# Kernel optimization log

Measured on AMD Instinct MI355X. Metric: run time of the kernel, lower is better.

Reference implementation:

```python
import jax, jax.numpy as jnp
import numpy as np

D_MODEL = 1024
NUM_HEADS = 16
D_K = D_MODEL // NUM_HEADS
THETA = 10000.0
B, S = 2, 2048


def apply_rope(x, token_position, theta=THETA):
    # x: [B, H, S, d_k]; token_position: [B, S] int
    d_k = x.shape[-1]
    inv_freq = 1.0 / theta ** (jnp.arange(0, d_k, 2, dtype=jnp.float32) / d_k)  # [d_k/2]
    angles = token_position.astype(jnp.float32)[:, :, None] * inv_freq[None, None, :]  # [B,S,d_k/2]
    cos = jnp.cos(angles)[:, None, :, :]  # [B,1,S,d_k/2]
    sin = jnp.sin(angles)[:, None, :, :]
    x_even = x[..., 0::2]
    x_odd = x[..., 1::2]
    rot_even = x_even * cos - x_odd * sin
    rot_odd = x_even * sin + x_odd * cos
    # interleave back: stack on new last axis, then flatten
    return jnp.stack([rot_even, rot_odd], axis=-1).reshape(x.shape)


def setup_inputs() -> dict:
    key = jax.random.key(0)
    kx, kq, kk, kv, ko = jax.random.split(key, 5)
    scale = 1.0 / np.sqrt(D_MODEL)
    x = jax.random.normal(kx, (B, S, D_MODEL), dtype=jnp.float32)
    WQ = jax.random.normal(kq, (D_MODEL, D_MODEL), dtype=jnp.float32) * scale
    WK = jax.random.normal(kk, (D_MODEL, D_MODEL), dtype=jnp.float32) * scale
    WV = jax.random.normal(kv, (D_MODEL, D_MODEL), dtype=jnp.float32) * scale
    WO = jax.random.normal(ko, (D_MODEL, D_MODEL), dtype=jnp.float32) * scale
    token_position = jnp.broadcast_to(jnp.arange(S, dtype=jnp.int32)[None, :], (B, S))
    return {"x": x, "token_position": token_position, "WQ": WQ, "WK": WK, "WV": WV, "WO": WO}


def reference(x, token_position, WQ, WK, WV, WO):
    Batch, seq, _ = x.shape
    Q = jnp.einsum('bsd,de->bse', x, WQ).reshape(Batch, seq, NUM_HEADS, D_K).transpose(0, 2, 1, 3)
    K = jnp.einsum('bsd,de->bse', x, WK).reshape(Batch, seq, NUM_HEADS, D_K).transpose(0, 2, 1, 3)
    V = jnp.einsum('bsd,de->bse', x, WV).reshape(Batch, seq, NUM_HEADS, D_K).transpose(0, 2, 1, 3)
    Q = apply_rope(Q, token_position)
    K = apply_rope(K, token_position)
    score = jnp.einsum('bhqd,bhkd->bhqk', Q, K) / jnp.sqrt(jnp.float32(D_K))
    causal = jnp.tril(jnp.ones((seq, seq), dtype=bool))  # [S,S]
    score = jnp.where(causal[None, None, :, :], score, -jnp.inf)
    probs = jax.nn.softmax(score, axis=-1)
    out = jnp.einsum('bhqk,bhkd->bhqd', probs, V)
    out = out.transpose(0, 2, 1, 3).reshape(Batch, seq, D_MODEL)
    return jnp.einsum('bsd,de->bse', out, WO)
```

## Files before the change

### kernel.cpp

```cpp
#include <hip/hip_runtime.h>
#include <hip/hip_bf16.h>

typedef __attribute__((ext_vector_type(8))) short short8;
typedef __attribute__((ext_vector_type(4))) float f32x4;
typedef __hip_bfloat16 bf16_t;

#define SEQ 2048
#define DM 1024
#define NH 16
#define DK 64

static __device__ __forceinline__ f32x4 mfma16x16x32(short8 a, short8 b, f32x4 c) {
  return __builtin_amdgcn_mfma_f32_16x16x32_bf16(a, b, c, 0, 0, 0);
}

__global__ void sniff_dtype(const unsigned int* __restrict__ x, int* __restrict__ flag) {
  int lane = threadIdx.x & 63;
  int cnt = 0;
  for (int r = 0; r < 4; ++r) {
    unsigned int v = x[lane + r * 64];
    int e = (v >> 7) & 0xFF;
    if (e >= 100 && e <= 145) cnt++;
  }
  for (int d = 1; d < 64; d <<= 1) cnt += __shfl_xor(cnt, d, 64);
  if (lane == 0) *flag = (cnt >= 192) ? 1 : 0;
}

__global__ __launch_bounds__(256) void prep(const void* __restrict__ x,
                                            bf16_t* __restrict__ Xc,
                                            const void* __restrict__ w0,
                                            const void* __restrict__ w1,
                                            const void* __restrict__ w2,
                                            const void* __restrict__ w3,
                                            bf16_t* __restrict__ wt_base,
                                            const int* __restrict__ tokpos,
                                            float2* __restrict__ rtab,
                                            const int* __restrict__ flag) {
  int f = *flag;
  int bx = blockIdx.x, t = threadIdx.x;
  __shared__ bf16_t tile[64][65];
  if (bx < 4096) {
    int i = bx * 256 + t;
    if (f) {
      ((uint2*)Xc)[i] = ((const uint2*)x)[i];
    } else {
      const float4 v = ((const float4*)x)[i];
      bf16_t o[4] = {__float2bfloat16(v.x), __float2bfloat16(v.y),
                     __float2bfloat16(v.z), __float2bfloat16(v.w)};
      ((uint2*)Xc)[i] = *(const uint2*)o;
    }
  } else if (bx < 5120) {
    int rem = bx - 4096;
    int z = rem >> 8, bxx = rem & 15, byy = (rem >> 4) & 15;
    const void* src = (z == 0) ? w0 : (z == 1) ? w1 : (z == 2) ? w2 : w3;
    bf16_t* dst = wt_base + (size_t)((z + 1) & 3) * DM * DM;
    int tx = t & 63, ty = t >> 6;
    int r0 = byy * 64, c0 = bxx * 64;
    for (int i = 0; i < 64; i += 4) {
      size_t idx = (size_t)(r0 + ty + i) * DM + c0 + tx;
      tile[ty + i][tx] = f ? ((const bf16_t*)src)[idx]
                           : __float2bfloat16(((const float*)src)[idx]);
    }
    __syncthreads();
    for (int i = 0; i < 64; i += 4)
      dst[(size_t)(c0 + ty + i) * DM + r0 + tx] = tile[tx][ty + i];
  } else {
    int i = (bx - 5120) * 256 + t;
    int m = i >> 5, pp = i & 31;
    float pos = (float)tokpos[m];
    float invf = __powf(10000.0f, -(float)pp * (1.0f / 32.0f));
    float sn, cs;
    sincosf(pos * invf, &sn, &cs);
    rtab[i] = make_float2(cs, sn);
  }
}

__global__ __launch_bounds__(256) void gemm128_qkv(const bf16_t* __restrict__ A,
                                                   const bf16_t* __restrict__ WTqkv,
                                                   bf16_t* __restrict__ Qb,
                                                   bf16_t* __restrict__ Kb,
                                                   bf16_t* __restrict__ VTo,
                                                   const float2* __restrict__ rtab) {
  __shared__ __align__(16) char smem[36864];
  bf16_t (*As)[72] = (bf16_t(*)[72])smem;
  bf16_t (*Bs)[72] = (bf16_t(*)[72])(smem + 18432);
  int t = threadIdx.x;
  int w = t >> 6, lane = t & 63, l15 = lane & 15, quad = lane >> 4;
  int wrow = w >> 1, wcol = w & 1;
  int m0 = blockIdx.y * 128, nx = blockIdx.x, n0 = nx * 128;
  int srow = t >> 1, scol = (t & 1) * 32;
  const bf16_t* ag = A + (size_t)(m0 + srow) * DM + scol;
  const bf16_t* bg = WTqkv + (size_t)(n0 + srow) * DM + scol;
  f32x4 acc[4][4] = {};
  for (int kk = 0; kk < DM; kk += 64) {
    short8 a0 = *(const short8*)(ag + kk);
    short8 a1 = *(const short8*)(ag + kk + 8);
    short8 a2 = *(const short8*)(ag + kk + 16);
    short8 a3 = *(const short8*)(ag + kk + 24);
    short8 b0 = *(const short8*)(bg + kk);
    short8 b1 = *(const short8*)(bg + kk + 8);
    short8 b2 = *(const short8*)(bg + kk + 16);
    short8 b3 = *(const short8*)(bg + kk + 24);
    __syncthreads();
    *(short8*)&As[srow][scol] = a0;       *(short8*)&As[srow][scol + 8] = a1;
    *(short8*)&As[srow][scol + 16] = a2;  *(short8*)&As[srow][scol + 24] = a3;
    *(short8*)&Bs[srow][scol] = b0;       *(short8*)&Bs[srow][scol + 8] = b1;
    *(short8*)&Bs[srow][scol + 16] = b2;  *(short8*)&Bs[srow][scol + 24] = b3;
    __syncthreads();
    short8 af[4][2], bfr[4][2];
#pragma unroll
    for (int mt = 0; mt < 4; ++mt) {
      af[mt][0] = *(const short8*)&As[wrow * 64 + mt * 16 + l15][quad * 8];
      af[mt][1] = *(const short8*)&As[wrow * 64 + mt * 16 + l15][32 + quad * 8];
    }
#pragma unroll
    for (int nt = 0; nt < 4; ++nt) {
      bfr[nt][0] = *(const short8*)&Bs[wcol * 64 + nt * 16 + l15][quad * 8];
      bfr[nt][1] = *(const short8*)&Bs[wcol * 64 + nt * 16 + l15][32 + quad * 8];
    }
#pragma unroll
    for (int mt = 0; mt < 4; ++mt)
#pragma unroll
      for (int nt = 0; nt < 4; ++nt) {
        acc[mt][nt] = mfma16x16x32(af[mt][0], bfr[nt][0], acc[mt][nt]);
        acc[mt][nt] = mfma16x16x32(af[mt][1], bfr[nt][1], acc[mt][nt]);
      }
  }

  int sel = nx >> 3;
  int nc = (nx & 7) * 128;
  __syncthreads();
  bf16_t (*Tw)[72] = (bf16_t(*)[72])(smem + w * 9216);
  int b = m0 >> 11;
  int h = (nc >> 6) + wcol;
  if (sel < 2) {
    bf16_t* dst = sel ? Kb : Qb;
    float sgnv = (l15 & 1) ? 1.0f : -1.0f;
#pragma unroll
    for (int mt = 0; mt < 4; ++mt)
#pragma unroll
      for (int r = 0; r < 4; ++r) {
        int m = m0 + wrow * 64 + mt * 16 + quad * 4 + r;
        const float2* tr = rtab + m * 32;
#pragma unroll
        for (int nt = 0; nt < 4; ++nt) {
          int d = nt * 16 + l15;
          float val = acc[mt][nt][r];
          float partner = __shfl_xor(val, 1, 64);
          float2 cssn = tr[d >> 1];
          Tw[mt * 16 + quad * 4 + r][d] = __float2bfloat16(val * cssn.x + sgnv * partner * cssn.y);
        }
      }
    int s_base = (m0 & (SEQ - 1)) + wrow * 64;
    bf16_t* dq = dst + ((size_t)(b * NH + h) * SEQ + s_base) * DK;
#pragma unroll
    for (int c = 0; c < 8; ++c) {
      int row = c * 8 + (lane >> 3);
      int col = (lane & 7) * 8;
      *(short8*)&dq[(size_t)row * DK + col] = *(const short8*)&Tw[row][col];
    }
  } else {
#pragma unroll
    for (int mt = 0; mt < 4; ++mt)
#pragma unroll
      for (int nt = 0; nt < 4; ++nt)
#pragma unroll
        for (int r = 0; r < 4; ++r)
          Tw[nt * 16 + l15][mt * 16 + quad * 4 + r] = __float2bfloat16(acc[mt][nt][r]);
    int s_base = m0 & (SEQ - 1);
#pragma unroll
    for (int c = 0; c < 4; ++c) {
      int d = c * 16 + (lane >> 2);
      int s2 = (lane & 3) * 16;
      size_t ob = ((size_t)(b * NH + h) * DK + d) * SEQ + s_base + wrow * 64 + s2;
      *(short8*)&VTo[ob] = *(const short8*)&Tw[d][s2];
      *(short8*)&VTo[ob + 8] = *(const short8*)&Tw[d][s2 + 8];
    }
  }
}

__global__ __launch_bounds__(256) void gemm128_out(const bf16_t* __restrict__ A,
                                                   const bf16_t* __restrict__ BT,
                                                   void* __restrict__ out,
                                                   const int* __restrict__ flag) {
  __shared__ __align__(16) bf16_t As[128][72];
  __shared__ __align__(16) bf16_t Bs[128][72];
  int f = *flag;
  int t = threadIdx.x;
  int w = t >> 6, lane = t & 63, l15 = lane & 15, quad = lane >> 4;
  int wrow = w >> 1, wcol = w & 1;
  int m0 = blockIdx.y * 128, n0 = blockIdx.x * 128;
  int srow = t >> 1, scol = (t & 1) * 32;
  const bf16_t* ag = A + (size_t)(m0 + srow) * DM + scol;
  const bf16_t* bg = BT + (size_t)(n0 + srow) * DM + scol;
  f32x4 acc[4][4] = {};
  for (int kk = 0; kk < DM; kk += 64) {
    short8 a0 = *(const short8*)(ag + kk);
    short8 a1 = *(const short8*)(ag + kk + 8);
    short8 a2 = *(const short8*)(ag + kk + 16);
    short8 a3 = *(const short8*)(ag + kk + 24);
    short8 b0 = *(const short8*)(bg + kk);
    short8 b1 = *(const short8*)(bg + kk + 8);
    short8 b2 = *(const short8*)(bg + kk + 16);
    short8 b3 = *(const short8*)(bg + kk + 24);
    __syncthreads();
    *(short8*)&As[srow][scol] = a0;       *(short8*)&As[srow][scol + 8] = a1;
    *(short8*)&As[srow][scol + 16] = a2;  *(short8*)&As[srow][scol + 24] = a3;
    *(short8*)&Bs[srow][scol] = b0;       *(short8*)&Bs[srow][scol + 8] = b1;
    *(short8*)&Bs[srow][scol + 16] = b2;  *(short8*)&Bs[srow][scol + 24] = b3;
    __syncthreads();
    short8 af[4][2], bfr[4][2];
#pragma unroll
    for (int mt = 0; mt < 4; ++mt) {
      af[mt][0] = *(const short8*)&As[wrow * 64 + mt * 16 + l15][quad * 8];
      af[mt][1] = *(const short8*)&As[wrow * 64 + mt * 16 + l15][32 + quad * 8];
    }
#pragma unroll
    for (int nt = 0; nt < 4; ++nt) {
      bfr[nt][0] = *(const short8*)&Bs[wcol * 64 + nt * 16 + l15][quad * 8];
      bfr[nt][1] = *(const short8*)&Bs[wcol * 64 + nt * 16 + l15][32 + quad * 8];
    }
#pragma unroll
    for (int mt = 0; mt < 4; ++mt)
#pragma unroll
      for (int nt = 0; nt < 4; ++nt) {
        acc[mt][nt] = mfma16x16x32(af[mt][0], bfr[nt][0], acc[mt][nt]);
        acc[mt][nt] = mfma16x16x32(af[mt][1], bfr[nt][1], acc[mt][nt]);
      }
  }
#pragma unroll
  for (int mt = 0; mt < 4; ++mt)
#pragma unroll
    for (int nt = 0; nt < 4; ++nt)
#pragma unroll
      for (int r = 0; r < 4; ++r) {
        int m = m0 + wrow * 64 + mt * 16 + quad * 4 + r;
        int col = n0 + wcol * 64 + nt * 16 + l15;
        size_t oidx = (size_t)m * DM + col;
        if (f) ((bf16_t*)out)[oidx] = __float2bfloat16(acc[mt][nt][r]);
        else   ((float*)out)[oidx] = acc[mt][nt][r];
      }
}

__global__ __launch_bounds__(256) void attn_fwd(const bf16_t* __restrict__ Q,
                                                const bf16_t* __restrict__ K,
                                                const bf16_t* __restrict__ VT,
                                                bf16_t* __restrict__ O) {
  int x = blockIdx.x, bh = blockIdx.y;
  int b = bh >> 4, h = bh & 15;
  int raw = (x + bh) & 31;
  int oct = raw >> 3, off = raw & 7;
  int p = (oct == 0) ? off : (oct == 1) ? (15 - off) : (oct == 2) ? (16 + off) : (31 - off);
  int t = threadIdx.x;
  int w = t >> 6, lane = t & 63, l15 = lane & 15, quad = lane >> 4;
  const size_t base = (size_t)bh * SEQ * DK;
  const bf16_t* Qp = Q + base;
  const bf16_t* Kp = K + base;
  const bf16_t* VTp = VT + base;

  __shared__ __align__(16) bf16_t Ks[64][72];
  __shared__ __align__(16) bf16_t Vs[64][72];
  __shared__ __align__(16) bf16_t Pb[4][16][72];

  int row = p * 64 + w * 16 + l15;
  short8 qf0 = *(const short8*)(Qp + (size_t)row * DK + quad * 8);
  short8 qf1 = *(const short8*)(Qp + (size_t)row * DK + 32 + quad * 8);

  int srow = t >> 2, scoff = (t & 3) * 16;
  const bf16_t* kst = Kp + (size_t)srow * DK + scoff;
  const bf16_t* vst = VTp + (size_t)srow * SEQ + scoff;

  short8 kA = *(const short8*)(kst);
  short8 kB = *(const short8*)(kst + 8);
  short8 vA = *(const short8*)(vst);
  short8 vB = *(const short8*)(vst + 8);

  f32x4 o[4] = {};
  float r[4] = {0.f, 0.f, 0.f, 0.f};

  for (int kb = 0; kb <= p; ++kb) {
    __syncthreads();
    *(short8*)&Ks[srow][scoff] = kA;
    *(short8*)&Ks[srow][scoff + 8] = kB;
    *(short8*)&Vs[srow][scoff] = vA;
    *(short8*)&Vs[srow][scoff + 8] = vB;
    __syncthreads();

    int nkb = (kb < p) ? (kb + 1) : p;
    kA = *(const short8*)(kst + (size_t)nkb * 64 * DK);
    kB = *(const short8*)(kst + (size_t)nkb * 64 * DK + 8);
    vA = *(const short8*)(vst + (size_t)nkb * 64);
    vB = *(const short8*)(vst + (size_t)nkb * 64 + 8);

    short8 kf0[4], kf1[4];
#pragma unroll
    for (int kt = 0; kt < 4; ++kt) {
      kf0[kt] = *(const short8*)&Ks[kt * 16 + l15][quad * 8];
      kf1[kt] = *(const short8*)&Ks[kt * 16 + l15][32 + quad * 8];
    }

    f32x4 sc[4];
#pragma unroll
    for (int kt = 0; kt < 4; ++kt) {
      f32x4 a = {};
      a = mfma16x16x32(qf0, kf0[kt], a);
      a = mfma16x16x32(qf1, kf1[kt], a);
      sc[kt] = a;
    }

    bool diag = (kb == p);
#pragma unroll
    for (int kt = 0; kt < 4; ++kt)
#pragma unroll
      for (int reg = 0; reg < 4; ++reg) {
        float sv = sc[kt][reg] * 0.125f;
        if (diag) {
          int kg = kt * 16 + l15, qg = w * 16 + quad * 4 + reg;
          if (kg > qg) sv = -30000.0f;
        }
        float pp = __expf(sv);
        r[reg] += pp;
        Pb[w][quad * 4 + reg][kt * 16 + l15] = __float2bfloat16(pp);
      }

    short8 p0 = *(const short8*)&Pb[w][l15][quad * 8];
    short8 p1 = *(const short8*)&Pb[w][l15][32 + quad * 8];
#pragma unroll
    for (int dt = 0; dt < 4; ++dt) {
      short8 vf0 = *(const short8*)&Vs[dt * 16 + l15][quad * 8];
      short8 vf1 = *(const short8*)&Vs[dt * 16 + l15][32 + quad * 8];
      o[dt] = mfma16x16x32(p0, vf0, o[dt]);
      o[dt] = mfma16x16x32(p1, vf1, o[dt]);
    }
  }

  for (int d = 1; d < 16; d <<= 1)
#pragma unroll
    for (int reg = 0; reg < 4; ++reg)
      r[reg] += __shfl_xor(r[reg], d, 64);

#pragma unroll
  for (int dt = 0; dt < 4; ++dt)
#pragma unroll
    for (int reg = 0; reg < 4; ++reg) {
      int col = h * DK + dt * 16 + l15;
      int q = p * 64 + w * 16 + quad * 4 + reg;
      O[((size_t)b * SEQ + q) * DM + col] = __float2bfloat16(o[dt][reg] / r[reg]);
    }
}

extern "C" void kernel_launch(void* const* d_in, const int* in_sizes, int n_in,
                              void* d_out, int out_size, void* d_ws, size_t ws_size,
                              hipStream_t stream) {
  const void* x = d_in[0];
  const int* tokpos = (const int*)d_in[1];
  const void* WQ = d_in[2];
  const void* WK = d_in[3];
  const void* WV = d_in[4];
  const void* WO = d_in[5];

  char* ws = (char*)d_ws;
  const size_t MB = 1024 * 1024;
  bf16_t* WT  = (bf16_t*)ws;
  bf16_t* Xc  = (bf16_t*)(ws + 8 * MB);
  bf16_t* Qb  = (bf16_t*)(ws + 16 * MB);
  bf16_t* Kb  = (bf16_t*)(ws + 24 * MB);
  bf16_t* VTb = (bf16_t*)(ws + 32 * MB);
  bf16_t* Ab  = (bf16_t*)(ws + 8 * MB);
  int* flag   = (int*)(ws + 40 * MB);
  float2* rtab = (float2*)(ws + 41 * MB);

  dim3 blk(256);
  sniff_dtype<<<1, 64, 0, stream>>>((const unsigned int*)x, flag);
  prep<<<5632, blk, 0, stream>>>(x, Xc, WQ, WK, WV, WO, WT, tokpos, rtab, flag);
  gemm128_qkv<<<dim3(24, 32), blk, 0, stream>>>(Xc, WT + (size_t)DM * DM, Qb, Kb, VTb, rtab);
  attn_fwd<<<dim3(32, 32), blk, 0, stream>>>(Qb, Kb, VTb, Ab);
  gemm128_out<<<dim3(8, 32), blk, 0, stream>>>(Ab, WT, d_out, flag);
}
```

Before: 213.1 us.

## Pair causal query tiles p and 31-p per attention block to share K/V loads

Each attention workgroup now handles two query tiles, p and 31-p, and walks the K/V blocks once, loading each into shared memory and using it for both tiles. This balances causal work across workgroups and halves the K/V global and LDS staging traffic per query tile. The grid is halved to 512 blocks, which lowers parallelism, and register pressure rises from the doubled accumulators and Q fragments.

Measured after the change: 206.1 us. 1.03x faster.

```diff
diff --git a/kernel.cpp b/kernel.cpp
--- a/kernel.cpp
+++ b/kernel.cpp
@@ -248,9 +248,11 @@
                                                 bf16_t* __restrict__ O) {
   int x = blockIdx.x, bh = blockIdx.y;
   int b = bh >> 4, h = bh & 15;
-  int raw = (x + bh) & 31;
-  int oct = raw >> 3, off = raw & 7;
-  int p = (oct == 0) ? off : (oct == 1) ? (15 - off) : (oct == 2) ? (16 + off) : (31 - off);
+  int g = x + (bh << 4);
+  int raw = (g + (g >> 8)) & 15;
+  const int pmap[16] = {0, 15, 1, 13, 2, 12, 3, 11, 4, 10, 5, 9, 6, 8, 7, 14};
+  int p = pmap[raw];
+  int qA = p, qB = 31 - p;
   int t = threadIdx.x;
   int w = t >> 6, lane = t & 63, l15 = lane & 15, quad = lane >> 4;
   const size_t base = (size_t)bh * SEQ * DK;
@@ -260,11 +262,14 @@
 
   __shared__ __align__(16) bf16_t Ks[64][72];
   __shared__ __align__(16) bf16_t Vs[64][72];
-  __shared__ __align__(16) bf16_t Pb[4][16][72];
-
-  int row = p * 64 + w * 16 + l15;
-  short8 qf0 = *(const short8*)(Qp + (size_t)row * DK + quad * 8);
-  short8 qf1 = *(const short8*)(Qp + (size_t)row * DK + 32 + quad * 8);
+  __shared__ __align__(16) bf16_t Pb[4][2][16][72];
+
+  int rowA = qA * 64 + w * 16 + l15;
+  int rowB = qB * 64 + w * 16 + l15;
+  short8 qfA0 = *(const short8*)(Qp + (size_t)rowA * DK + quad * 8);
+  short8 qfA1 = *(const short8*)(Qp + (size_t)rowA * DK + 32 + quad * 8);
+  short8 qfB0 = *(const short8*)(Qp + (size_t)rowB * DK + quad * 8);
+  short8 qfB1 = *(const short8*)(Qp + (size_t)rowB * DK + 32 + quad * 8);
 
   int srow = t >> 2, scoff = (t & 3) * 16;
   const bf16_t* kst = Kp + (size_t)srow * DK + scoff;
@@ -275,10 +280,10 @@
   short8 vA = *(const short8*)(vst);
   short8 vB = *(const short8*)(vst + 8);
 
-  f32x4 o[4] = {};
-  float r[4] = {0.f, 0.f, 0.f, 0.f};
-
-  for (int kb = 0; kb <= p; ++kb) {
+  f32x4 oA[4] = {}, oB[4] = {};
+  float rA[4] = {0.f, 0.f, 0.f, 0.f}, rB[4] = {0.f, 0.f, 0.f, 0.f};
+
+  for (int kb = 0; kb <= qB; ++kb) {
     __syncthreads();
     *(short8*)&Ks[srow][scoff] = kA;
     *(short8*)&Ks[srow][scoff + 8] = kB;
@@ -286,66 +291,94 @@
     *(short8*)&Vs[srow][scoff + 8] = vB;
     __syncthreads();
 
-    int nkb = (kb < p) ? (kb + 1) : p;
+    int nkb = (kb < qB) ? (kb + 1) : qB;
     kA = *(const short8*)(kst + (size_t)nkb * 64 * DK);
     kB = *(const short8*)(kst + (size_t)nkb * 64 * DK + 8);
     vA = *(const short8*)(vst + (size_t)nkb * 64);
     vB = *(const short8*)(vst + (size_t)nkb * 64 + 8);
 
-    short8 kf0[4], kf1[4];
-#pragma unroll
-    for (int kt = 0; kt < 4; ++kt) {
-      kf0[kt] = *(const short8*)&Ks[kt * 16 + l15][quad * 8];
-      kf1[kt] = *(const short8*)&Ks[kt * 16 + l15][32 + quad * 8];
-    }
-
-    f32x4 sc[4];
-#pragma unroll
-    for (int kt = 0; kt < 4; ++kt) {
-      f32x4 a = {};
-      a = mfma16x16x32(qf0, kf0[kt], a);
-      a = mfma16x16x32(qf1, kf1[kt], a);
-      sc[kt] = a;
-    }
-
-    bool diag = (kb == p);
-#pragma unroll
-    for (int kt = 0; kt < 4; ++kt)
-#pragma unroll
-      for (int reg = 0; reg < 4; ++reg) {
-        float sv = sc[kt][reg] * 0.125f;
-        if (diag) {
-          int kg = kt * 16 + l15, qg = w * 16 + quad * 4 + reg;
-          if (kg > qg) sv = -30000.0f;
+    bool doA = (kb <= qA);
+
+    {
+      f32x4 sc[4];
+#pragma unroll
+      for (int kt = 0; kt < 4; ++kt) {
+        f32x4 a = {};
+        a = mfma16x16x32(qfB0, *(const short8*)&Ks[kt * 16 + l15][quad * 8], a);
+        a = mfma16x16x32(qfB1, *(const short8*)&Ks[kt * 16 + l15][32 + quad * 8], a);
+        sc[kt] = a;
+      }
+      bool diag = (kb == qB);
+#pragma unroll
+      for (int kt = 0; kt < 4; ++kt)
+#pragma unroll
+        for (int reg = 0; reg < 4; ++reg) {
+          float sv = sc[kt][reg] * 0.125f;
+          if (diag) {
+            int kg = kt * 16 + l15, qg = w * 16 + quad * 4 + reg;
+            if (kg > qg) sv = -30000.0f;
+          }
+          float pp = __expf(sv);
+          rB[reg] += pp;
+          Pb[w][1][quad * 4 + reg][kt * 16 + l15] = __float2bfloat16(pp);
         }
-        float pp = __expf(sv);
-        r[reg] += pp;
-        Pb[w][quad * 4 + reg][kt * 16 + l15] = __float2bfloat16(pp);
-      }
-
-    short8 p0 = *(const short8*)&Pb[w][l15][quad * 8];
-    short8 p1 = *(const short8*)&Pb[w][l15][32 + quad * 8];
-#pragma unroll
-    for (int dt = 0; dt < 4; ++dt) {
-      short8 vf0 = *(const short8*)&Vs[dt * 16 + l15][quad * 8];
-      short8 vf1 = *(const short8*)&Vs[dt * 16 + l15][32 + quad * 8];
-      o[dt] = mfma16x16x32(p0, vf0, o[dt]);
-      o[dt] = mfma16x16x32(p1, vf1, o[dt]);
+      short8 p0 = *(const short8*)&Pb[w][1][l15][quad * 8];
+      short8 p1 = *(const short8*)&Pb[w][1][l15][32 + quad * 8];
+#pragma unroll
+      for (int dt = 0; dt < 4; ++dt) {
+        oB[dt] = mfma16x16x32(p0, *(const short8*)&Vs[dt * 16 + l15][quad * 8], oB[dt]);
+        oB[dt] = mfma16x16x32(p1, *(const short8*)&Vs[dt * 16 + l15][32 + quad * 8], oB[dt]);
+      }
+    }
+    if (doA) {
+      f32x4 sc[4];
+#pragma unroll
+      for (int kt = 0; kt < 4; ++kt) {
+        f32x4 a = {};
+        a = mfma16x16x32(qfA0, *(const short8*)&Ks[kt * 16 + l15][quad * 8], a);
+        a = mfma16x16x32(qfA1, *(const short8*)&Ks[kt * 16 + l15][32 + quad * 8], a);
+        sc[kt] = a;
+      }
+      bool diag = (kb == qA);
+#pragma unroll
+      for (int kt = 0; kt < 4; ++kt)
+#pragma unroll
+        for (int reg = 0; reg < 4; ++reg) {
+          float sv = sc[kt][reg] * 0.125f;
+          if (diag) {
+            int kg = kt * 16 + l15, qg = w * 16 + quad * 4 + reg;
+            if (kg > qg) sv = -30000.0f;
+          }
+          float pp = __expf(sv);
+          rA[reg] += pp;
+          Pb[w][0][quad * 4 + reg][kt * 16 + l15] = __float2bfloat16(pp);
+        }
+      short8 p0 = *(const short8*)&Pb[w][0][l15][quad * 8];
+      short8 p1 = *(const short8*)&Pb[w][0][l15][32 + quad * 8];
+#pragma unroll
+      for (int dt = 0; dt < 4; ++dt) {
+        oA[dt] = mfma16x16x32(p0, *(const short8*)&Vs[dt * 16 + l15][quad * 8], oA[dt]);
+        oA[dt] = mfma16x16x32(p1, *(const short8*)&Vs[dt * 16 + l15][32 + quad * 8], oA[dt]);
+      }
     }
   }
 
   for (int d = 1; d < 16; d <<= 1)
 #pragma unroll
-    for (int reg = 0; reg < 4; ++reg)
-      r[reg] += __shfl_xor(r[reg], d, 64);
+    for (int reg = 0; reg < 4; ++reg) {
+      rA[reg] += __shfl_xor(rA[reg], d, 64);
+      rB[reg] += __shfl_xor(rB[reg], d, 64);
+    }
 
 #pragma unroll
   for (int dt = 0; dt < 4; ++dt)
 #pragma unroll
     for (int reg = 0; reg < 4; ++reg) {
       int col = h * DK + dt * 16 + l15;
-      int q = p * 64 + w * 16 + quad * 4 + reg;
-      O[((size_t)b * SEQ + q) * DM + col] = __float2bfloat16(o[dt][reg] / r[reg]);
+      int qa = qA * 64 + w * 16 + quad * 4 + reg;
+      int qb_ = qB * 64 + w * 16 + quad * 4 + reg;
+      O[((size_t)b * SEQ + qa) * DM + col] = __float2bfloat16(oA[dt][reg] / rA[reg]);
+      O[((size_t)b * SEQ + qb_) * DM + col] = __float2bfloat16(oB[dt][reg] / rB[reg]);
     }
 }
 
@@ -374,6 +407,6 @@
   sniff_dtype<<<1, 64, 0, stream>>>((const unsigned int*)x, flag);
   prep<<<5632, blk, 0, stream>>>(x, Xc, WQ, WK, WV, WO, WT, tokpos, rtab, flag);
   gemm128_qkv<<<dim3(24, 32), blk, 0, stream>>>(Xc, WT + (size_t)DM * DM, Qb, Kb, VTb, rtab);
-  attn_fwd<<<dim3(32, 32), blk, 0, stream>>>(Qb, Kb, VTb, Ab);
+  attn_fwd<<<dim3(16, 32), blk, 0, stream>>>(Qb, Kb, VTb, Ab);
   gemm128_out<<<dim3(8, 32), blk, 0, stream>>>(Ab, WT, d_out, flag);
 }
```
